# Optimization experiments

Hardware: AMD Instinct MI355X
Metric: run time of the kernel (lower is better)

The kernel has to match this reference:

```python
import jax, jax.numpy as jnp
import numpy as np

EPS = 1e-5

def layer_norm(x, gamma, beta):
    mu = jnp.mean(x, axis=-1, keepdims=True)
    var = jnp.var(x, axis=-1, keepdims=True)
    return (x - mu) * jax.lax.rsqrt(var + EPS) * gamma + beta

def setup_inputs() -> dict:
    key = jax.random.key(0)
    ks = jax.random.split(key, 8)
    T, B, E, H, K = 2048, 2, 1024, 16, 64
    x = jax.random.normal(ks[0], (T, B, E), dtype=jnp.float32)
    # causal mask: 0 where allowed (s<=t), -1e9 where masked
    attn_mask = jnp.where(jnp.tril(jnp.ones((T, T), dtype=bool)), 0.0, -1e9).astype(jnp.float32)
    def xavier(k, shape, gain):
        fan_out, fan_in = shape
        std = gain * np.sqrt(2.0 / (fan_in + fan_out))
        return (jax.random.normal(k, shape, dtype=jnp.float32) * std)
    Wq = xavier(ks[1], (H * K, E), 1.0)
    Wk = xavier(ks[2], (K, E), 1.0)
    Wv = xavier(ks[3], (E, E), 1.0)
    return {
        'x': x, 'attn_mask': attn_mask,
        'Wq': Wq, 'bq': jnp.zeros((H * K,), jnp.float32),
        'Wk': Wk, 'bk': jnp.zeros((K,), jnp.float32),
        'Wv': Wv, 'bv': jnp.zeros((E,), jnp.float32),
        'k_gamma': jnp.ones((K,), jnp.float32), 'k_beta': jnp.zeros((K,), jnp.float32),
        'v_gamma': jnp.ones((E,), jnp.float32), 'v_beta': jnp.zeros((E,), jnp.float32),
    }

def reference(x, attn_mask, Wq, bq, Wk, bk, Wv, bv, k_gamma, k_beta, v_gamma, v_beta):
    T, B, E = x.shape
    K = Wk.shape[0]
    H = Wq.shape[0] // K
    q = (x @ Wq.T + bq).reshape(T, B, H, K)          # [T,B,H,K]
    k = layer_norm(x @ Wk.T + bk, k_gamma, k_beta)   # [T,B,K]
    v = layer_norm(x @ Wv.T + bv, v_gamma, v_beta)   # [T,B,E]
    # outer-product state per step, then causal cumulative sum.
    # einsum('ts,sbkd->tbkd', scaling*causal_mask, s) == cumsum over s<=t,
    # scaled per query position t by (t+1)^-0.5 (mask is causal lower-tri).
    outer = jnp.einsum('tbk,tbd->tbkd', k, v)        # [T,B,K,E]
    s = jnp.cumsum(outer, axis=0)
    scaling = jax.lax.rsqrt(jnp.arange(1, T + 1, dtype=x.dtype))
    s = s * scaling[:, None, None, None]
    qn = jnp.mean(jax.nn.softmax(q, axis=-1), axis=2)  # [T,B,K] (dropout_p=0, eval)
    attn = jnp.einsum('tbk,tbkd->tbd', qn, s)          # [T,B,E]
    return attn
```

## Files before the change

### kernel.cpp

```cpp
#include <hip/hip_runtime.h>
#include <math.h>

#define T_DIM 2048
#define B_DIM 2
#define E_DIM 1024
#define K_DIM 64
#define H_DIM 16
#define R_DIM (T_DIM * B_DIM)
#define WROWS 2176
#define NTILE 136

typedef __bf16 bf16x8 __attribute__((ext_vector_type(8)));
typedef __bf16 bf16x4 __attribute__((ext_vector_type(4)));
typedef float f32x4 __attribute__((ext_vector_type(4)));

__global__ __launch_bounds__(256) void cvt_all(const float* __restrict__ X,
                                               const float* __restrict__ Wq,
                                               const float* __restrict__ Wv,
                                               const float* __restrict__ Wk,
                                               __bf16* __restrict__ XB,
                                               __bf16* __restrict__ WB) {
    const size_t nq = (size_t)1024 * 1024;
    const size_t nk = (size_t)64 * 1024;
    bf16x8 o;
    if (blockIdx.x < 2048) {
        size_t g = ((size_t)blockIdx.x * 256 + threadIdx.x) * 8;
        float4 a = *(const float4*)&X[g];
        float4 b = *(const float4*)&X[g + 4];
        o[0] = (__bf16)a.x; o[1] = (__bf16)a.y; o[2] = (__bf16)a.z; o[3] = (__bf16)a.w;
        o[4] = (__bf16)b.x; o[5] = (__bf16)b.y; o[6] = (__bf16)b.z; o[7] = (__bf16)b.w;
        *(bf16x8*)&XB[g] = o;
    } else {
        size_t g = ((size_t)(blockIdx.x - 2048) * 256 + threadIdx.x) * 8;
        if (g < 2 * nq + nk) {
            const float* src;
            size_t off;
            if (g < nq)          { src = Wq; off = g; }
            else if (g < 2 * nq) { src = Wv; off = g - nq; }
            else                 { src = Wk; off = g - 2 * nq; }
            float4 a = *(const float4*)&src[off];
            float4 b = *(const float4*)&src[off + 4];
            o[0] = (__bf16)a.x; o[1] = (__bf16)a.y; o[2] = (__bf16)a.z; o[3] = (__bf16)a.w;
            o[4] = (__bf16)b.x; o[5] = (__bf16)b.y; o[6] = (__bf16)b.z; o[7] = (__bf16)b.w;
        } else {
#pragma unroll
            for (int i = 0; i < 8; ++i) o[i] = (__bf16)0.f;
        }
        *(bf16x8*)&WB[g] = o;
    }
}

__global__ __launch_bounds__(256) void gemm_mfma(const __bf16* __restrict__ XB,
                                                 const __bf16* __restrict__ WB,
                                                 const float* __restrict__ bq,
                                                 const float* __restrict__ bv,
                                                 const float* __restrict__ bk,
                                                 __bf16* __restrict__ Qb,
                                                 __bf16* __restrict__ Vb,
                                                 float* __restrict__ Kr) {
    __shared__ __bf16 Als[128 * 32];
    __shared__ __bf16 Bls[128 * 32];
    const int tid = threadIdx.x;
    const int lane = tid & 63;
    const int w = tid >> 6;
    const int wm = (w & 1) * 64;
    const int wn = (w >> 1) * 64;
    const int rBase = blockIdx.x * 128;
    const int cBase = blockIdx.y * 128;

    const int c0 = tid, c1 = tid + 256;
    const __bf16* gA0 = XB + (size_t)(rBase + (c0 >> 2)) * E_DIM + (c0 & 3) * 8;
    const __bf16* gA1 = XB + (size_t)(rBase + (c1 >> 2)) * E_DIM + (c1 & 3) * 8;
    const __bf16* gB0 = WB + (size_t)(cBase + (c0 >> 2)) * E_DIM + (c0 & 3) * 8;
    const __bf16* gB1 = WB + (size_t)(cBase + (c1 >> 2)) * E_DIM + (c1 & 3) * 8;
    __bf16* lA0 = Als + c0 * 8;
    __bf16* lA1 = Als + c1 * 8;
    __bf16* lB0 = Bls + c0 * 8;
    __bf16* lB1 = Bls + c1 * 8;

    const int fr = lane & 15;
    const int fk = (lane >> 4) * 8;
    const __bf16* aF = Als + (wm + fr) * 32 + fk;
    const __bf16* bF = Bls + (wn + fr) * 32 + fk;

    f32x4 acc[4][4] = {};

    for (int kk = 0; kk < E_DIM; kk += 32) {
        __syncthreads();
        __builtin_amdgcn_global_load_lds(
            (const __attribute__((address_space(1))) void*)(gA0 + kk),
            (__attribute__((address_space(3))) void*)lA0, 16, 0, 0);
        __builtin_amdgcn_global_load_lds(
            (const __attribute__((address_space(1))) void*)(gA1 + kk),
            (__attribute__((address_space(3))) void*)lA1, 16, 0, 0);
        __builtin_amdgcn_global_load_lds(
            (const __attribute__((address_space(1))) void*)(gB0 + kk),
            (__attribute__((address_space(3))) void*)lB0, 16, 0, 0);
        __builtin_amdgcn_global_load_lds(
            (const __attribute__((address_space(1))) void*)(gB1 + kk),
            (__attribute__((address_space(3))) void*)lB1, 16, 0, 0);
        __syncthreads();

        bf16x8 af[4], bfr[4];
#pragma unroll
        for (int mt = 0; mt < 4; ++mt) af[mt] = *(const bf16x8*)(aF + mt * 16 * 32);
#pragma unroll
        for (int nt = 0; nt < 4; ++nt) bfr[nt] = *(const bf16x8*)(bF + nt * 16 * 32);
#pragma unroll
        for (int mt = 0; mt < 4; ++mt)
#pragma unroll
            for (int nt = 0; nt < 4; ++nt)
                acc[mt][nt] = __builtin_amdgcn_mfma_f32_16x16x32_bf16(
                    af[mt], bfr[nt], acc[mt][nt], 0, 0, 0);
    }

    const int row0 = rBase + wm + (lane >> 4) * 4;
    if (cBase < 2048) {
        const float* bias;
        __bf16* Cout;
        int colBase;
        if (cBase < 1024) { bias = bq; Cout = Qb; colBase = cBase; }
        else              { bias = bv; Cout = Vb; colBase = cBase - 1024; }
        const int col0 = colBase + wn + (lane & 15);
#pragma unroll
        for (int mt = 0; mt < 4; ++mt)
#pragma unroll
            for (int nt = 0; nt < 4; ++nt) {
                int cc = col0 + nt * 16;
                float bb = bias[cc];
#pragma unroll
                for (int r = 0; r < 4; ++r)
                    Cout[(size_t)(row0 + mt * 16 + r) * E_DIM + cc] =
                        (__bf16)(acc[mt][nt][r] + bb);
            }
    } else {
        const int col0 = wn + (lane & 15);
#pragma unroll
        for (int mt = 0; mt < 4; ++mt)
#pragma unroll
            for (int nt = 0; nt < 4; ++nt) {
                int cc = col0 + nt * 16;
                if (cc < 64) {
                    float bb = bk[cc];
#pragma unroll
                    for (int r = 0; r < 4; ++r)
                        Kr[(size_t)(row0 + mt * 16 + r) * K_DIM + cc] =
                            acc[mt][nt][r] + bb;
                }
            }
    }
}

__global__ __launch_bounds__(256) void rowops(const __bf16* __restrict__ Qb,
                                              const float* __restrict__ Kraw,
                                              const __bf16* __restrict__ Vb,
                                              const float* __restrict__ kg,
                                              const float* __restrict__ kb,
                                              __bf16* __restrict__ QNB,
                                              __bf16* __restrict__ KNB,
                                              float2* __restrict__ ST) {
    const int r = blockIdx.x;
    const int tid = threadIdx.x;
    const int lane = tid & 63, wv = tid >> 6;
    const int t = r >> 1, b = r & 1;
    __shared__ float redq[4][64];
    __shared__ float redv[2][4];

    float acc = 0.f;
#pragma unroll
    for (int h4 = 0; h4 < 4; ++h4) {
        int h = wv * 4 + h4;
        float v = (float)Qb[(size_t)r * 1024 + h * 64 + lane];
        float m = v;
#pragma unroll
        for (int off = 32; off; off >>= 1) m = fmaxf(m, __shfl_xor(m, off));
        float e = expf(v - m);
        float ssum = e;
#pragma unroll
        for (int off = 32; off; off >>= 1) ssum += __shfl_xor(ssum, off);
        acc += e / ssum;
    }
    redq[wv][lane] = acc;

    {
        bf16x4 v4 = *(const bf16x4*)&Vb[(size_t)r * 1024 + tid * 4];
        float a = (float)v4[0], c = (float)v4[1], d = (float)v4[2], e = (float)v4[3];
        float s = a + c + d + e;
        float s2 = a * a + c * c + d * d + e * e;
#pragma unroll
        for (int off = 32; off; off >>= 1) {
            s += __shfl_xor(s, off);
            s2 += __shfl_xor(s2, off);
        }
        if (lane == 0) { redv[0][wv] = s; redv[1][wv] = s2; }
    }
    __syncthreads();

    if (tid < 64) {
        float s = redq[0][tid] + redq[1][tid] + redq[2][tid] + redq[3][tid];
        QNB[((size_t)b * T_DIM + t) * K_DIM + tid] = (__bf16)(s * (1.f / 16.f));
    } else if (tid < 128) {
        float v = Kraw[(size_t)r * K_DIM + lane];
        float s = v, s2 = v * v;
#pragma unroll
        for (int off = 32; off; off >>= 1) {
            s += __shfl_xor(s, off);
            s2 += __shfl_xor(s2, off);
        }
        float mean = s * (1.f / 64.f);
        float var = s2 * (1.f / 64.f) - mean * mean;
        float inv = rsqrtf(var + 1e-5f);
        KNB[((size_t)b * T_DIM + t) * K_DIM + lane] =
            (__bf16)((v - mean) * inv * kg[lane] + kb[lane]);
    } else if (tid == 128) {
        float s = redv[0][0] + redv[0][1] + redv[0][2] + redv[0][3];
        float s2 = redv[1][0] + redv[1][1] + redv[1][2] + redv[1][3];
        float mean = s * (1.f / 1024.f);
        float var = s2 * (1.f / 1024.f) - mean * mean;
        ST[r] = make_float2(mean, rsqrtf(var + 1e-5f));
    }
}

__global__ __launch_bounds__(256) void transpose_lnv(const __bf16* __restrict__ VB,
                                                     const float2* __restrict__ ST,
                                                     const float* __restrict__ gamma,
                                                     const float* __restrict__ beta,
                                                     __bf16* __restrict__ VT) {
    __shared__ float tile[64][65];
    const int tb = blockIdx.x, eb = blockIdx.y, b = blockIdx.z;
    const int tid = threadIdx.x;
#pragma unroll
    for (int j = 0; j < 2; ++j) {
        int idx = tid + j * 256;
        int tl = idx >> 3, e8 = idx & 7;
        int r = (tb * 64 + tl) * B_DIM + b;
        float2 st = ST[r];
        bf16x8 v = *(const bf16x8*)&VB[(size_t)r * E_DIM + eb * 64 + e8 * 8];
#pragma unroll
        for (int i = 0; i < 8; ++i)
            tile[tl][e8 * 8 + i] = ((float)v[i] - st.x) * st.y;
    }
    __syncthreads();
#pragma unroll
    for (int j = 0; j < 4; ++j) {
        int idx = tid + j * 256;
        int e = idx >> 4, t4 = idx & 15;
        float g = gamma[eb * 64 + e], bb = beta[eb * 64 + e];
        bf16x4 o;
#pragma unroll
        for (int i = 0; i < 4; ++i) o[i] = (__bf16)(tile[t4 * 4 + i][e] * g + bb);
        *(bf16x4*)&VT[((size_t)b * E_DIM + eb * 64 + e) * T_DIM + tb * 64 + t4 * 4] = o;
    }
}

__global__ __launch_bounds__(256) void scoreK(const __bf16* __restrict__ QNB,
                                              const __bf16* __restrict__ KNB,
                                              __bf16* __restrict__ Pg) {
    __shared__ __bf16 qns[128 * 72];
    __shared__ __bf16 kns[128 * 72];
    const int tileId = blockIdx.x;
    const int b = blockIdx.y;
    int qt = 0, rem = tileId;
    while (rem > qt) { rem -= (qt + 1); ++qt; }
    const int st = rem;
    const int tid = threadIdx.x;
    const int lane = tid & 63;
    const int w = tid >> 6;
    const int qL = lane & 15;
    const int quad = lane >> 4;

    const __bf16* qsrc = QNB + ((size_t)b * T_DIM + qt * 128) * K_DIM;
    const __bf16* ksrc = KNB + ((size_t)b * T_DIM + st * 128) * K_DIM;
#pragma unroll
    for (int j = 0; j < 4; ++j) {
        int idx = tid + j * 256;
        int row = idx >> 3, k8 = idx & 7;
        *(bf16x8*)&qns[row * 72 + k8 * 8] = *(const bf16x8*)&qsrc[row * K_DIM + k8 * 8];
        *(bf16x8*)&kns[row * 72 + k8 * 8] = *(const bf16x8*)&ksrc[row * K_DIM + k8 * 8];
    }
    __syncthreads();

    f32x4 acc[8][2] = {};
#pragma unroll
    for (int kit = 0; kit < 2; ++kit) {
        bf16x8 bfr[2];
#pragma unroll
        for (int nt = 0; nt < 2; ++nt) {
            int q = w * 32 + nt * 16 + qL;
            bfr[nt] = *(const bf16x8*)&qns[q * 72 + kit * 32 + quad * 8];
        }
#pragma unroll
        for (int mt = 0; mt < 8; ++mt) {
            bf16x8 af = *(const bf16x8*)&kns[(mt * 16 + qL) * 72 + kit * 32 + quad * 8];
#pragma unroll
            for (int nt = 0; nt < 2; ++nt)
                acc[mt][nt] = __builtin_amdgcn_mfma_f32_16x16x32_bf16(
                    af, bfr[nt], acc[mt][nt], 0, 0, 0);
        }
    }
    __bf16* pb = Pg + ((size_t)(b * NTILE + tileId)) * 128 * 128;
#pragma unroll
    for (int mt = 0; mt < 8; ++mt)
#pragma unroll
        for (int nt = 0; nt < 2; ++nt) {
            int q = w * 32 + nt * 16 + qL;
            int s0 = mt * 16 + quad * 4;
            bf16x4 o;
#pragma unroll
            for (int r = 0; r < 4; ++r) {
                float val = acc[mt][nt][r];
                if (qt == st && (s0 + r) > q) val = 0.f;
                o[r] = (__bf16)val;
            }
            *(bf16x4*)&pb[(size_t)q * 128 + s0] = o;
        }
}

__global__ __launch_bounds__(256) void flashPV(const __bf16* __restrict__ Pg,
                                               const __bf16* __restrict__ VT,
                                               float* __restrict__ OUT) {
    __shared__ __align__(16) __bf16 vts[64 * 136];
    __shared__ __align__(16) __bf16 ps[128 * 136];
    const int p = blockIdx.x;
    const int es = blockIdx.y;
    const int b = blockIdx.z;
    const int tid = threadIdx.x;
    const int lane = tid & 63;
    const int w = tid >> 6;
    const int qL = lane & 15;
    const int quad = lane >> 4;

    for (int ph = 0; ph < 2; ++ph) {
        const int qt = ph ? (15 - p) : p;
        const int tileBase = qt * (qt + 1) / 2;
        f32x4 acc[4][2] = {};

        for (int st = 0; st <= qt; ++st) {
            __syncthreads();
#pragma unroll
            for (int j = 0; j < 4; ++j) {
                int idx = tid + j * 256;
                int e = idx >> 4, sc = idx & 15;
                *(bf16x8*)&vts[e * 136 + sc * 8] =
                    *(const bf16x8*)&VT[((size_t)b * E_DIM + es * 64 + e) * T_DIM +
                                        st * 128 + sc * 8];
            }
            const __bf16* pb = Pg + ((size_t)(b * NTILE + tileBase + st)) * 128 * 128;
#pragma unroll
            for (int j = 0; j < 8; ++j) {
                int idx = tid + j * 256;
                int q = idx >> 4, sc = idx & 15;
                *(bf16x8*)&ps[q * 136 + sc * 8] = *(const bf16x8*)&pb[q * 128 + sc * 8];
            }
            __syncthreads();
#pragma unroll
            for (int kit = 0; kit < 4; ++kit) {
                bf16x8 bfr[2];
#pragma unroll
                for (int nt = 0; nt < 2; ++nt) {
                    int q = w * 32 + nt * 16 + qL;
                    bfr[nt] = *(const bf16x8*)&ps[q * 136 + kit * 32 + quad * 8];
                }
#pragma unroll
                for (int mt = 0; mt < 4; ++mt) {
                    bf16x8 af = *(const bf16x8*)&vts[(mt * 16 + qL) * 136 + kit * 32 + quad * 8];
#pragma unroll
                    for (int nt = 0; nt < 2; ++nt)
                        acc[mt][nt] = __builtin_amdgcn_mfma_f32_16x16x32_bf16(
                            af, bfr[nt], acc[mt][nt], 0, 0, 0);
                }
            }
        }
        __syncthreads();

        float* tb = (float*)vts + w * 640;
#pragma unroll
        for (int mt = 0; mt < 4; ++mt) {
#pragma unroll
            for (int nt = 0; nt < 2; ++nt)
                *(f32x4*)&tb[(nt * 16 + qL) * 20 + quad * 4] = acc[mt][nt];
#pragma unroll
            for (int j = 0; j < 2; ++j) {
                int fid = lane + j * 64;
                int q = fid >> 2, e4 = fid & 3;
                float4 val = *(const float4*)&tb[q * 20 + e4 * 4];
                int t = qt * 128 + w * 32 + q;
                float sca = rsqrtf((float)(t + 1));
                float4 r = {val.x * sca, val.y * sca, val.z * sca, val.w * sca};
                *(float4*)&OUT[((size_t)t * B_DIM + b) * E_DIM + es * 64 + mt * 16 + e4 * 4] = r;
            }
        }
    }
}

extern "C" void kernel_launch(void* const* d_in, const int* in_sizes, int n_in,
                              void* d_out, int out_size, void* d_ws,
                              size_t ws_size, hipStream_t stream) {
    const float* x = (const float*)d_in[0];
    const float* Wq = (const float*)d_in[2];
    const float* bq = (const float*)d_in[3];
    const float* Wk = (const float*)d_in[4];
    const float* bk = (const float*)d_in[5];
    const float* Wv = (const float*)d_in[6];
    const float* bv = (const float*)d_in[7];
    const float* kg = (const float*)d_in[8];
    const float* kb = (const float*)d_in[9];
    const float* vg = (const float*)d_in[10];
    const float* vb = (const float*)d_in[11];
    float* out = (float*)d_out;

    char* base = (char*)d_ws;
    const size_t MB = 1024 * 1024;
    __bf16* qb    = (__bf16*)(base + 0);
    __bf16* vbuf  = (__bf16*)(base + 8 * MB);
    float*  kraw  = (float*)(base + 16 * MB);
    __bf16* xb    = (__bf16*)(base + 17 * MB);
    __bf16* wb    = (__bf16*)(base + 25 * MB);
    __bf16* qnb   = (__bf16*)(base + 30 * MB);
    __bf16* knb   = (__bf16*)(base + 31 * MB);
    float2* stats = (float2*)(base + 32 * MB);
    __bf16* Pg  = (__bf16*)(base + 0);
    __bf16* vbT = xb;

    cvt_all<<<dim3(2048 + WROWS * 1024 / 2048), 256, 0, stream>>>(x, Wq, Wv, Wk, xb, wb);
    gemm_mfma<<<dim3(32, 17), 256, 0, stream>>>(xb, wb, bq, bv, bk, qb, vbuf, kraw);
    rowops<<<dim3(R_DIM), 256, 0, stream>>>(qb, kraw, vbuf, kg, kb, qnb, knb, stats);
    transpose_lnv<<<dim3(T_DIM / 64, E_DIM / 64, B_DIM), 256, 0, stream>>>(
        vbuf, stats, vg, vb, vbT);
    scoreK<<<dim3(NTILE, B_DIM), 256, 0, stream>>>(qnb, knb, Pg);
    flashPV<<<dim3(8, 16, B_DIM), 256, 0, stream>>>(Pg, vbT, out);
}
```

Measured before the change: 186.6 us.

## Shrink projection GEMM N-tile to 64 and register-prefetch next tile in flashPV

The projection GEMM now uses 128x64 tiles (grid 32x33) instead of 128x128 (32x17). This removes the wasted work on the padded K block, where only 64 of 128 columns were used, and gives more blocks to fill the GPU. flashPV now loads the next V/P tile into registers while the MFMA loop runs on the current tile in LDS, so global latency overlaps compute. The cost is more registers per thread and lower arithmetic intensity in the GEMM.

```diff
diff --git a/kernel.cpp b/kernel.cpp
--- a/kernel.cpp
+++ b/kernel.cpp
@@ -13,6 +13,11 @@
 typedef __bf16 bf16x8 __attribute__((ext_vector_type(8)));
 typedef __bf16 bf16x4 __attribute__((ext_vector_type(4)));
 typedef float f32x4 __attribute__((ext_vector_type(4)));
+
+#define GLD16(gptr, lptr)                                                      \
+    __builtin_amdgcn_global_load_lds(                                          \
+        (const __attribute__((address_space(1))) void*)(gptr),                 \
+        (__attribute__((address_space(3))) void*)(lptr), 16, 0, 0)
 
 __global__ __launch_bounds__(256) void cvt_all(const float* __restrict__ X,
                                                const float* __restrict__ Wq,
@@ -59,74 +64,63 @@
                                                  __bf16* __restrict__ Vb,
                                                  float* __restrict__ Kr) {
     __shared__ __bf16 Als[128 * 32];
-    __shared__ __bf16 Bls[128 * 32];
+    __shared__ __bf16 Bls[64 * 32];
     const int tid = threadIdx.x;
     const int lane = tid & 63;
     const int w = tid >> 6;
     const int wm = (w & 1) * 64;
-    const int wn = (w >> 1) * 64;
+    const int wn = (w >> 1) * 32;
     const int rBase = blockIdx.x * 128;
-    const int cBase = blockIdx.y * 128;
-
-    const int c0 = tid, c1 = tid + 256;
-    const __bf16* gA0 = XB + (size_t)(rBase + (c0 >> 2)) * E_DIM + (c0 & 3) * 8;
-    const __bf16* gA1 = XB + (size_t)(rBase + (c1 >> 2)) * E_DIM + (c1 & 3) * 8;
-    const __bf16* gB0 = WB + (size_t)(cBase + (c0 >> 2)) * E_DIM + (c0 & 3) * 8;
-    const __bf16* gB1 = WB + (size_t)(cBase + (c1 >> 2)) * E_DIM + (c1 & 3) * 8;
-    __bf16* lA0 = Als + c0 * 8;
-    __bf16* lA1 = Als + c1 * 8;
-    __bf16* lB0 = Bls + c0 * 8;
-    __bf16* lB1 = Bls + c1 * 8;
+    const int cBase = blockIdx.y * 64;
+
+    const int cA0 = tid, cA1 = tid + 256;
+    const __bf16* gA0 = XB + (size_t)(rBase + (cA0 >> 2)) * E_DIM + (cA0 & 3) * 8;
+    const __bf16* gA1 = XB + (size_t)(rBase + (cA1 >> 2)) * E_DIM + (cA1 & 3) * 8;
+    const __bf16* gB0 = WB + (size_t)(cBase + (tid >> 2)) * E_DIM + (tid & 3) * 8;
+    __bf16* lA0 = Als + cA0 * 8;
+    __bf16* lA1 = Als + cA1 * 8;
+    __bf16* lB0 = Bls + tid * 8;
 
     const int fr = lane & 15;
     const int fk = (lane >> 4) * 8;
     const __bf16* aF = Als + (wm + fr) * 32 + fk;
     const __bf16* bF = Bls + (wn + fr) * 32 + fk;
 
-    f32x4 acc[4][4] = {};
+    f32x4 acc[4][2] = {};
 
     for (int kk = 0; kk < E_DIM; kk += 32) {
         __syncthreads();
-        __builtin_amdgcn_global_load_lds(
-            (const __attribute__((address_space(1))) void*)(gA0 + kk),
-            (__attribute__((address_space(3))) void*)lA0, 16, 0, 0);
-        __builtin_amdgcn_global_load_lds(
-            (const __attribute__((address_space(1))) void*)(gA1 + kk),
-            (__attribute__((address_space(3))) void*)lA1, 16, 0, 0);
-        __builtin_amdgcn_global_load_lds(
-            (const __attribute__((address_space(1))) void*)(gB0 + kk),
-            (__attribute__((address_space(3))) void*)lB0, 16, 0, 0);
-        __builtin_amdgcn_global_load_lds(
-            (const __attribute__((address_space(1))) void*)(gB1 + kk),
-            (__attribute__((address_space(3))) void*)lB1, 16, 0, 0);
+        GLD16(gA0 + kk, lA0);
+        GLD16(gA1 + kk, lA1);
+        GLD16(gB0 + kk, lB0);
         __syncthreads();
 
-        bf16x8 af[4], bfr[4];
+        bf16x8 af[4], bfr[2];
 #pragma unroll
         for (int mt = 0; mt < 4; ++mt) af[mt] = *(const bf16x8*)(aF + mt * 16 * 32);
 #pragma unroll
-        for (int nt = 0; nt < 4; ++nt) bfr[nt] = *(const bf16x8*)(bF + nt * 16 * 32);
+        for (int nt = 0; nt < 2; ++nt) bfr[nt] = *(const bf16x8*)(bF + nt * 16 * 32);
 #pragma unroll
         for (int mt = 0; mt < 4; ++mt)
 #pragma unroll
-            for (int nt = 0; nt < 4; ++nt)
+            for (int nt = 0; nt < 2; ++nt)
                 acc[mt][nt] = __builtin_amdgcn_mfma_f32_16x16x32_bf16(
                     af[mt], bfr[nt], acc[mt][nt], 0, 0, 0);
     }
 
     const int row0 = rBase + wm + (lane >> 4) * 4;
+    const int colLoc = wn + (lane & 15);
     if (cBase < 2048) {
         const float* bias;
         __bf16* Cout;
         int colBase;
         if (cBase < 1024) { bias = bq; Cout = Qb; colBase = cBase; }
         else              { bias = bv; Cout = Vb; colBase = cBase - 1024; }
-        const int col0 = colBase + wn + (lane & 15);
 #pragma unroll
         for (int mt = 0; mt < 4; ++mt)
 #pragma unroll
-            for (int nt = 0; nt < 4; ++nt) {
-                int cc = col0 + nt * 16;
+            for (int nt = 0; nt < 2; ++nt) {
+                int cc = colBase + colLoc + nt * 16;
                 float bb = bias[cc];
 #pragma unroll
                 for (int r = 0; r < 4; ++r)
@@ -134,19 +128,16 @@
                         (__bf16)(acc[mt][nt][r] + bb);
             }
     } else {
-        const int col0 = wn + (lane & 15);
 #pragma unroll
         for (int mt = 0; mt < 4; ++mt)
 #pragma unroll
-            for (int nt = 0; nt < 4; ++nt) {
-                int cc = col0 + nt * 16;
-                if (cc < 64) {
-                    float bb = bk[cc];
-#pragma unroll
-                    for (int r = 0; r < 4; ++r)
-                        Kr[(size_t)(row0 + mt * 16 + r) * K_DIM + cc] =
-                            acc[mt][nt][r] + bb;
-                }
+            for (int nt = 0; nt < 2; ++nt) {
+                int cc = colLoc + nt * 16;
+                float bb = bk[cc];
+#pragma unroll
+                for (int r = 0; r < 4; ++r)
+                    Kr[(size_t)(row0 + mt * 16 + r) * K_DIM + cc] =
+                        acc[mt][nt][r] + bb;
             }
     }
 }
@@ -330,29 +321,60 @@
     const int qL = lane & 15;
     const int quad = lane >> 4;
 
+    const __bf16* vtBase = VT + ((size_t)b * E_DIM + es * 64) * T_DIM;
+
     for (int ph = 0; ph < 2; ++ph) {
         const int qt = ph ? (15 - p) : p;
         const int tileBase = qt * (qt + 1) / 2;
         f32x4 acc[4][2] = {};
-
-        for (int st = 0; st <= qt; ++st) {
-            __syncthreads();
-#pragma unroll
-            for (int j = 0; j < 4; ++j) {
-                int idx = tid + j * 256;
-                int e = idx >> 4, sc = idx & 15;
-                *(bf16x8*)&vts[e * 136 + sc * 8] =
-                    *(const bf16x8*)&VT[((size_t)b * E_DIM + es * 64 + e) * T_DIM +
-                                        st * 128 + sc * 8];
-            }
-            const __bf16* pb = Pg + ((size_t)(b * NTILE + tileBase + st)) * 128 * 128;
+        bf16x8 vreg[4], preg[8];
+
+#pragma unroll
+        for (int j = 0; j < 4; ++j) {
+            int idx = tid + j * 256;
+            int e = idx >> 4, sc = idx & 15;
+            vreg[j] = *(const bf16x8*)&vtBase[(size_t)e * T_DIM + sc * 8];
+        }
+        {
+            const __bf16* pb = Pg + ((size_t)(b * NTILE + tileBase)) * 128 * 128;
 #pragma unroll
             for (int j = 0; j < 8; ++j) {
                 int idx = tid + j * 256;
                 int q = idx >> 4, sc = idx & 15;
-                *(bf16x8*)&ps[q * 136 + sc * 8] = *(const bf16x8*)&pb[q * 128 + sc * 8];
-            }
-            __syncthreads();
+                preg[j] = *(const bf16x8*)&pb[q * 128 + sc * 8];
+            }
+        }
+        __syncthreads();
+#pragma unroll
+        for (int j = 0; j < 4; ++j) {
+            int idx = tid + j * 256;
+            *(bf16x8*)&vts[(idx >> 4) * 136 + (idx & 15) * 8] = vreg[j];
+        }
+#pragma unroll
+        for (int j = 0; j < 8; ++j) {
+            int idx = tid + j * 256;
+            *(bf16x8*)&ps[(idx >> 4) * 136 + (idx & 15) * 8] = preg[j];
+        }
+        __syncthreads();
+
+        for (int st = 0; st <= qt; ++st) {
+            if (st < qt) {
+#pragma unroll
+                for (int j = 0; j < 4; ++j) {
+                    int idx = tid + j * 256;
+                    int e = idx >> 4, sc = idx & 15;
+                    vreg[j] = *(const bf16x8*)&vtBase[(size_t)e * T_DIM +
+                                                      (st + 1) * 128 + sc * 8];
+                }
+                const __bf16* pb =
+                    Pg + ((size_t)(b * NTILE + tileBase + st + 1)) * 128 * 128;
+#pragma unroll
+                for (int j = 0; j < 8; ++j) {
+                    int idx = tid + j * 256;
+                    int q = idx >> 4, sc = idx & 15;
+                    preg[j] = *(const bf16x8*)&pb[q * 128 + sc * 8];
+                }
+            }
 #pragma unroll
             for (int kit = 0; kit < 4; ++kit) {
                 bf16x8 bfr[2];
@@ -369,6 +391,20 @@
                         acc[mt][nt] = __builtin_amdgcn_mfma_f32_16x16x32_bf16(
                             af, bfr[nt], acc[mt][nt], 0, 0, 0);
                 }
+            }
+            if (st < qt) {
+                __syncthreads();
+#pragma unroll
+                for (int j = 0; j < 4; ++j) {
+                    int idx = tid + j * 256;
+                    *(bf16x8*)&vts[(idx >> 4) * 136 + (idx & 15) * 8] = vreg[j];
+                }
+#pragma unroll
+                for (int j = 0; j < 8; ++j) {
+                    int idx = tid + j * 256;
+                    *(bf16x8*)&ps[(idx >> 4) * 136 + (idx & 15) * 8] = preg[j];
+                }
+                __syncthreads();
             }
         }
         __syncthreads();
@@ -423,7 +459,7 @@
     __bf16* vbT = xb;
 
     cvt_all<<<dim3(2048 + WROWS * 1024 / 2048), 256, 0, stream>>>(x, Wq, Wv, Wk, xb, wb);
-    gemm_mfma<<<dim3(32, 17), 256, 0, stream>>>(xb, wb, bq, bv, bk, qb, vbuf, kraw);
+    gemm_mfma<<<dim3(32, 33), 256, 0, stream>>>(xb, wb, bq, bv, bk, qb, vbuf, kraw);
     rowops<<<dim3(R_DIM), 256, 0, stream>>>(qb, kraw, vbuf, kg, kb, qnb, knb, stats);
     transpose_lnv<<<dim3(T_DIM / 64, E_DIM / 64, B_DIM), 256, 0, stream>>>(
         vbuf, stats, vg, vb, vbT);
```

Result: no change. 189.0 us (+1.3%).
